# Optimization experiments

Hardware: AMD Instinct MI355X
Metric: run time of the kernel (lower is better)

Reference implementation:

```python
import jax, jax.numpy as jnp
import numpy as np

N = 50000        # nodes
E = 1000000      # edges
HID = 128        # hidden_dim
EA = 16          # edge_attr_dim
MLP_IN = 2 * HID + EA + 1   # dist + feat[row] + feat[col] + edge_attr = 273
WNUM = 3         # FullyConnectedTensorProduct(sh, 1x0e, sh) weight_numel = max_ell+1

# map each of the 9 SH components (l=0,1,2) to its l-path weight index
_L_IDX = jnp.array([0, 1, 1, 1, 2, 2, 2, 2, 2])


def _sh_lmax2(u):
    """e3nn real spherical harmonics, lmax=2, normalization='norm'.
    u: [E,3] unit vectors (e3nn x,y,z order); each l-block has unit L2 norm."""
    x, y, z = u[..., 0], u[..., 1], u[..., 2]
    s3 = jnp.sqrt(jnp.asarray(3.0, u.dtype))
    return jnp.stack([
        jnp.ones_like(x),                      # l=0
        x, y, z,                               # l=1 (unit vector)
        s3 * x * z,                            # l=2 (component / sqrt(5))
        s3 * x * y,
        y * y - 0.5 * (x * x + z * z),
        s3 * y * z,
        0.5 * s3 * (z * z - x * x),
    ], axis=-1)


def setup_inputs() -> dict:
    key = jax.random.key(0)
    ks = jax.random.split(key, 6)
    return {
        "node_feat": jax.random.normal(ks[0], (N, HID), jnp.float32),
        "node_pos": jax.random.normal(ks[1], (N, 3), jnp.float32),
        "edge_attr": jax.random.normal(ks[2], (E, EA), jnp.float32),
        "W1": jax.random.normal(ks[3], (MLP_IN, HID), jnp.float32) / np.sqrt(MLP_IN).astype(np.float32),
        "b1": jnp.zeros((HID,), jnp.float32),
        "W2": jax.random.normal(ks[4], (HID, WNUM), jnp.float32) / np.sqrt(HID).astype(np.float32),
        "b2": jnp.zeros((WNUM,), jnp.float32),
        "edge_index": jax.random.randint(ks[5], (2, E), 0, N),
    }


def reference(node_feat, node_pos, edge_attr, W1, b1, W2, b2, edge_index):
    row, col = edge_index[0], edge_index[1]
    diff = node_pos[row] - node_pos[col]                         # [E,3] gather
    dist = jnp.linalg.norm(diff, axis=-1, keepdims=True)         # [E,1]
    msg = jnp.concatenate([dist, node_feat[row], node_feat[col], edge_attr], axis=-1)
    h = jax.nn.silu(msg @ W1 + b1)                               # [E,HID]
    w = jax.nn.silu(h @ W2 + b2)                                 # [E,3] per-l TP weights (last_act=True)
    u = diff / jnp.maximum(dist, 1e-12)                          # normalize=True
    sh = jax.lax.stop_gradient(_sh_lmax2(u))                     # [E,9], .detach() in source
    # FullyConnectedTensorProduct(sh, ones '1x0e') with component irrep-norm and
    # element path-norm reduces exactly to scaling each l-block by its path weight.
    diff_sh = sh * w[:, _L_IDX]                                  # [E,9]
    # scatter-mean over destination `row`
    seg = jax.ops.segment_sum(diff_sh, row, num_segments=N)      # [N,9]
    cnt = jax.ops.segment_sum(jnp.ones((diff_sh.shape[0],), diff_sh.dtype), row, num_segments=N)
    return seg / jnp.maximum(cnt, 1.0)[:, None]
```

## Files before the change

kernel.cpp:

```cpp
#include <hip/hip_runtime.h>
#include <hip/hip_bf16.h>
#include <hip/hip_fp16.h>
#include <math.h>

#define HID 128
#define EA 16
#define BM 64
#define EAP 40
#define PQP 136
#define FTP 136
#define KT1 9
#define NC 8
#define NTHREADS 256
#define GRIDM 1536

#define HIST_OFF   0
#define WRPTR_OFF  (256*1024)
#define W1S_OFF    (512*1024)
#define W1S_ELEMS  (KT1 * NC * 64 * 8)
#define W2S_OFF    (W1S_OFF + W1S_ELEMS * 2)
#define W2S_ELEMS  (4 * 64 * 8)
#define SORTED_OFF (1024*1024)
#define FEAT16_OFF (SORTED_OFF + 8*1024*1024)
#define P_OFF      (FEAT16_OFF + 13*1024*1024)
#define Q_OFF      (P_OFF + 13*1024*1024)

typedef _Float16 half8 __attribute__((ext_vector_type(8)));
typedef _Float16 half4v __attribute__((ext_vector_type(4)));
typedef float floatx4 __attribute__((ext_vector_type(4)));
typedef unsigned long long u64;

__device__ __forceinline__ float silu_f(float x) {
    return x * (1.0f / (1.0f + __expf(-x)));
}

__global__ void prep_kernel(const float* __restrict__ W1,
                            const float* __restrict__ W2,
                            const float* __restrict__ node_feat,
                            _Float16* __restrict__ w1s,
                            _Float16* __restrict__ w2s,
                            _Float16* __restrict__ feat16,
                            float* __restrict__ seg,
                            int nf8, int nseg) {
    const int idx = blockIdx.x * NTHREADS + threadIdx.x;
    if (idx < W1S_ELEMS) {
        const int i    = idx & 7;
        const int lane = (idx >> 3) & 63;
        const int c    = (idx >> 9) & 7;
        const int kt   = idx >> 12;
        const int k    = kt * 32 + (lane >> 4) * 8 + i;
        const int n    = c * 16 + (lane & 15);
        float v = 0.0f;
        if (k < 273) {
            const int src = (k < 272) ? (k + 1) : 0;
            v = W1[src * HID + n];
        }
        w1s[idx] = (_Float16)v;
    }
    if (idx < W2S_ELEMS) {
        const int i    = idx & 7;
        const int lane = (idx >> 3) & 63;
        const int kt   = idx >> 9;
        const int k    = kt * 32 + (lane >> 4) * 8 + i;
        const int n    = lane & 15;
        const float v  = (n < 3) ? W2[k * 3 + n] : 0.0f;
        w2s[idx] = (_Float16)v;
    }
    if (idx < nf8) {
        const float4* src = (const float4*)node_feat;
        const float4 a = src[2 * idx];
        const float4 b = src[2 * idx + 1];
        half8 h = { (_Float16)a.x, (_Float16)a.y, (_Float16)a.z, (_Float16)a.w,
                    (_Float16)b.x, (_Float16)b.y, (_Float16)b.z, (_Float16)b.w };
        ((half8*)feat16)[idx] = h;
    }
    if (idx < nseg) seg[idx] = 0.0f;
}

__global__ void pq_kernel(const _Float16* __restrict__ feat16,
                          const _Float16* __restrict__ w1s,
                          _Float16* __restrict__ P,
                          _Float16* __restrict__ Q, int N) {
    __shared__ _Float16 ftile[BM][FTP];
    const int tid  = threadIdx.x;
    const int base = blockIdx.x * BM;
    const int m    = tid >> 2;
    const int sub  = tid & 3;
    const int node = base + m;
    const int ncl  = node < N ? node : 0;

    const half8* fr = (const half8*)(feat16 + (long)ncl * HID);
    #pragma unroll
    for (int t = 0; t < 4; ++t)
        *(half8*)(&ftile[m][sub * 32 + t * 8]) = fr[sub * 4 + t];
    __syncthreads();

    const int wave = tid >> 6, lane = tid & 63, lrow = lane & 15, g = lane >> 4;
    floatx4 aP[4][2], aQ[4][2];
    #pragma unroll
    for (int rb = 0; rb < 4; ++rb) {
        aP[rb][0] = (floatx4){0,0,0,0}; aP[rb][1] = (floatx4){0,0,0,0};
        aQ[rb][0] = (floatx4){0,0,0,0}; aQ[rb][1] = (floatx4){0,0,0,0};
    }
    #pragma unroll
    for (int kt = 0; kt < 4; ++kt) {
        const half8 bP0 = *(const half8*)(w1s + ((size_t)(((kt    ) * NC + 2*wave    ) * 64 + lane)) * 8);
        const half8 bP1 = *(const half8*)(w1s + ((size_t)(((kt    ) * NC + 2*wave + 1) * 64 + lane)) * 8);
        const half8 bQ0 = *(const half8*)(w1s + ((size_t)(((kt + 4) * NC + 2*wave    ) * 64 + lane)) * 8);
        const half8 bQ1 = *(const half8*)(w1s + ((size_t)(((kt + 4) * NC + 2*wave + 1) * 64 + lane)) * 8);
        #pragma unroll
        for (int rb = 0; rb < 4; ++rb) {
            const half8 af = *(const half8*)&ftile[16*rb + lrow][kt*32 + g*8];
            aP[rb][0] = __builtin_amdgcn_mfma_f32_16x16x32_f16(af, bP0, aP[rb][0], 0, 0, 0);
            aP[rb][1] = __builtin_amdgcn_mfma_f32_16x16x32_f16(af, bP1, aP[rb][1], 0, 0, 0);
            aQ[rb][0] = __builtin_amdgcn_mfma_f32_16x16x32_f16(af, bQ0, aQ[rb][0], 0, 0, 0);
            aQ[rb][1] = __builtin_amdgcn_mfma_f32_16x16x32_f16(af, bQ1, aQ[rb][1], 0, 0, 0);
        }
    }
    const int c0 = 32 * wave + lrow, c1 = c0 + 16;

    __syncthreads();
    #pragma unroll
    for (int rb = 0; rb < 4; ++rb)
        #pragma unroll
        for (int reg = 0; reg < 4; ++reg) {
            const int r = 16*rb + 4*g + reg;
            ftile[r][c0] = (_Float16)aP[rb][0][reg];
            ftile[r][c1] = (_Float16)aP[rb][1][reg];
        }
    __syncthreads();
    if (node < N) {
        #pragma unroll
        for (int t = 0; t < 4; ++t)
            *(half8*)(P + (long)node * HID + sub * 32 + t * 8) = *(half8*)&ftile[m][sub*32 + t*8];
    }
    __syncthreads();
    #pragma unroll
    for (int rb = 0; rb < 4; ++rb)
        #pragma unroll
        for (int reg = 0; reg < 4; ++reg) {
            const int r = 16*rb + 4*g + reg;
            ftile[r][c0] = (_Float16)aQ[rb][0][reg];
            ftile[r][c1] = (_Float16)aQ[rb][1][reg];
        }
    __syncthreads();
    if (node < N) {
        #pragma unroll
        for (int t = 0; t < 4; ++t)
            *(half8*)(Q + (long)node * HID + sub * 32 + t * 8) = *(half8*)&ftile[m][sub*32 + t*8];
    }
}

__global__ void hist_kernel(const int* __restrict__ edge_index,
                            int* __restrict__ hist, int E) {
    const int e = blockIdx.x * NTHREADS + threadIdx.x;
    if (e < E) atomicAdd(hist + edge_index[e], 1);
}

__global__ void scan_kernel(const int* __restrict__ hist,
                            int* __restrict__ wrptr, int N) {
    __shared__ int wsum[16];
    const int tid  = threadIdx.x;
    const int C    = (N + 1023) >> 10;
    int lo = tid * C; if (lo > N) lo = N;
    int hi = lo + C;  if (hi > N) hi = N;
    int s = 0;
    for (int i = lo; i < hi; ++i) s += hist[i];
    const int lane = tid & 63, wid = tid >> 6;
    int v = s;
    #pragma unroll
    for (int d = 1; d < 64; d <<= 1) {
        const int t = __shfl_up(v, d, 64);
        if (lane >= d) v += t;
    }
    if (lane == 63) wsum[wid] = v;
    __syncthreads();
    if (tid == 0) {
        int a = 0;
        #pragma unroll
        for (int w = 0; w < 16; ++w) { const int t = wsum[w]; wsum[w] = a; a += t; }
    }
    __syncthreads();
    int run = wsum[wid] + v - s;
    for (int i = lo; i < hi; ++i) { wrptr[i] = run; run += hist[i]; }
}

__global__ void permute_kernel(const int* __restrict__ edge_index,
                               int* __restrict__ wrptr,
                               u64* __restrict__ sorted, int E) {
    const int e = blockIdx.x * NTHREADS + threadIdx.x;
    if (e < E) {
        const int row = edge_index[e];
        const int col = edge_index[(long)E + e];
        const int p   = atomicAdd(wrptr + row, 1);
        sorted[p] = ((u64)(unsigned)e << 32)
                  | ((u64)(unsigned short)col << 16)
                  | (u64)(unsigned short)row;
    }
}

__global__ __launch_bounds__(NTHREADS, 6)
void edge_kernel(
    const _Float16* __restrict__ Pp,
    const _Float16* __restrict__ Qp,
    const float* __restrict__ node_pos,
    const float* __restrict__ edge_attr,
    const float* __restrict__ b1,
    const float* __restrict__ b2,
    const u64*   __restrict__ sorted,
    const _Float16* __restrict__ w1s,
    const _Float16* __restrict__ w2s,
    float* __restrict__ seg,
    int E, int ntiles)
{
    __shared__ _Float16 eat[BM][EAP];
    __shared__ _Float16 pq[BM][PQP];
    __shared__ float diffb[BM][4];
    __shared__ float wbuf[BM][3];
    __shared__ int   rowb[BM];

    const int tid  = threadIdx.x;
    const int m    = tid >> 2;
    const int sub  = tid & 3;
    const int wave = tid >> 6;
    const int lane = tid & 63;
    const int lrow = lane & 15;
    const int g    = lane >> 4;

    const half8 bW0 = *(const half8*)(w1s + ((size_t)((8 * NC + 2*wave    ) * 64 + lane)) * 8);
    const half8 bW1 = *(const half8*)(w1s + ((size_t)((8 * NC + 2*wave + 1) * 64 + lane)) * 8);
    const int col0 = 32 * wave + lrow, col1 = col0 + 16;
    const float bb0 = b1[col0], bb1 = b1[col1];

    for (int tile = blockIdx.x; tile < ntiles; tile += GRIDM) {
        __syncthreads();

        {
            const long p  = (long)tile * BM + m;
            const long pc = p < E ? p : (long)(E - 1);
            const u64 pk  = sorted[pc];
            const int row = (int)(pk & 0xffff);
            const int cn  = (int)((pk >> 16) & 0xffff);
            const unsigned e = (unsigned)(pk >> 32);

            const half8* Pr = (const half8*)(Pp + (long)row * HID);
            const half8* Qc = (const half8*)(Qp + (long)cn * HID);
            #pragma unroll
            for (int t = 0; t < 4; ++t) {
                const half8 a = Pr[sub * 4 + t];
                const half8 b = Qc[sub * 4 + t];
                half8 r;
                #pragma unroll
                for (int j = 0; j < 8; ++j)
                    r[j] = (_Float16)((float)a[j] + (float)b[j]);
                *(half8*)(&pq[m][sub * 32 + t * 8]) = r;
            }
            const float4 ea = ((const float4*)(edge_attr + (long)e * EA))[sub];
            half4v h4 = { (_Float16)ea.x, (_Float16)ea.y, (_Float16)ea.z, (_Float16)ea.w };
            *(half4v*)(&eat[m][sub * 4]) = h4;
            if (sub == 0) {
                rowb[m] = row;
                const float dx = node_pos[row*3+0] - node_pos[cn*3+0];
                const float dy = node_pos[row*3+1] - node_pos[cn*3+1];
                const float dz = node_pos[row*3+2] - node_pos[cn*3+2];
                const float dist = sqrtf(dx*dx + dy*dy + dz*dz);
                diffb[m][0] = dx; diffb[m][1] = dy; diffb[m][2] = dz; diffb[m][3] = dist;
                half8 z = { (_Float16)dist, (_Float16)0.f, (_Float16)0.f, (_Float16)0.f,
                            (_Float16)0.f, (_Float16)0.f, (_Float16)0.f, (_Float16)0.f };
                *(half8*)(&eat[m][16]) = z;
            } else if (sub == 1) {
                half8 z = { (_Float16)0.f, (_Float16)0.f, (_Float16)0.f, (_Float16)0.f,
                            (_Float16)0.f, (_Float16)0.f, (_Float16)0.f, (_Float16)0.f };
                *(half8*)(&eat[m][24]) = z;
            }
        }
        __syncthreads();

        floatx4 acc[4][2];
        #pragma unroll
        for (int rb = 0; rb < 4; ++rb) {
            acc[rb][0] = (floatx4){0,0,0,0};
            acc[rb][1] = (floatx4){0,0,0,0};
        }
        #pragma unroll
        for (int rb = 0; rb < 4; ++rb) {
            const half8 af = *(const half8*)&eat[16*rb + lrow][g * 8];
            acc[rb][0] = __builtin_amdgcn_mfma_f32_16x16x32_f16(af, bW0, acc[rb][0], 0, 0, 0);
            acc[rb][1] = __builtin_amdgcn_mfma_f32_16x16x32_f16(af, bW1, acc[rb][1], 0, 0, 0);
        }

        #pragma unroll
        for (int rb = 0; rb < 4; ++rb)
            #pragma unroll
            for (int reg = 0; reg < 4; ++reg) {
                const int r = 16*rb + 4*g + reg;
                const float h0 = silu_f(acc[rb][0][reg] + (float)pq[r][col0] + bb0);
                const float h1 = silu_f(acc[rb][1][reg] + (float)pq[r][col1] + bb1);
                pq[r][col0] = (_Float16)h0;
                pq[r][col1] = (_Float16)h1;
            }
        __syncthreads();

        {
            floatx4 acc2 = (floatx4){0,0,0,0};
            #pragma unroll
            for (int kt = 0; kt < 4; ++kt) {
                const half8 af = *(const half8*)&pq[16*wave + lrow][kt*32 + g*8];
                const half8 bf = *(const half8*)(w2s + ((size_t)(kt * 64 + lane)) * 8);
                acc2 = __builtin_amdgcn_mfma_f32_16x16x32_f16(af, bf, acc2, 0, 0, 0);
            }
            if (lrow < 3) {
                const float bb2 = b2[lrow];
                #pragma unroll
                for (int reg = 0; reg < 4; ++reg)
                    wbuf[16*wave + 4*g + reg][lrow] = silu_f(acc2[reg] + bb2);
            }
        }
        __syncthreads();

        if (tid < BM) {
            const long p = (long)tile * BM + tid;
            const bool valid = p < E;
            int rw = valid ? rowb[tid] : -1;
            float v[9];
            if (valid) {
                const float dx = diffb[tid][0], dy = diffb[tid][1], dz = diffb[tid][2];
                const float dist = diffb[tid][3];
                const float inv = 1.0f / fmaxf(dist, 1e-12f);
                const float x = dx * inv, y = dy * inv, z = dz * inv;
                const float s3 = 1.7320508075688772f;
                const float w0 = wbuf[tid][0], w1 = wbuf[tid][1], w2v = wbuf[tid][2];
                v[0] = w0;
                v[1] = x * w1; v[2] = y * w1; v[3] = z * w1;
                v[4] = s3 * x * z * w2v;
                v[5] = s3 * x * y * w2v;
                v[6] = (y * y - 0.5f * (x * x + z * z)) * w2v;
                v[7] = s3 * y * z * w2v;
                v[8] = 0.5f * s3 * (z * z - x * x) * w2v;
            } else {
                #pragma unroll
                for (int c = 0; c < 9; ++c) v[c] = 0.0f;
            }
            const int rprev = __shfl_up(rw, 1, 64);
            int fl = (tid == 0 || rw != rprev) ? 1 : 0;
            #pragma unroll
            for (int d = 1; d < 64; d <<= 1) {
                const int fo = __shfl_up(fl, d, 64);
                #pragma unroll
                for (int c = 0; c < 9; ++c) {
                    const float vo = __shfl_up(v[c], d, 64);
                    if (tid >= d && !fl) v[c] += vo;
                }
                if (tid >= d) fl |= fo;
            }
            const int rnext = __shfl_down(rw, 1, 64);
            const bool endseg = (tid == 63) || (rw != rnext);
            if (endseg && rw >= 0) {
                float* o = seg + (long)rw * 9;
                #pragma unroll
                for (int c = 0; c < 9; ++c) atomicAdd(o + c, v[c]);
            }
        }
    }
}

__global__ void finalize_kernel(float* __restrict__ out,
                                const int* __restrict__ hist, int n_out) {
    const int i = blockIdx.x * blockDim.x + threadIdx.x;
    if (i < n_out) {
        const float c = (float)hist[i / 9];
        out[i] = out[i] / fmaxf(c, 1.0f);
    }
}

extern "C" void kernel_launch(void* const* d_in, const int* in_sizes, int n_in,
                              void* d_out, int out_size, void* d_ws, size_t ws_size,
                              hipStream_t stream) {
    const float* node_feat  = (const float*)d_in[0];
    const float* node_pos   = (const float*)d_in[1];
    const float* edge_attr  = (const float*)d_in[2];
    const float* W1         = (const float*)d_in[3];
    const float* b1         = (const float*)d_in[4];
    const float* W2         = (const float*)d_in[5];
    const float* b2         = (const float*)d_in[6];
    const int*   edge_index = (const int*)d_in[7];

    const int E = in_sizes[7] / 2;
    const int N = in_sizes[1] / 3;
    const int ntiles = (E + BM - 1) / BM;

    char* ws = (char*)d_ws;
    float*    seg    = (float*)d_out;
    int*      hist   = (int*)(ws + HIST_OFF);
    int*      wrptr  = (int*)(ws + WRPTR_OFF);
    _Float16* w1s    = (_Float16*)(ws + W1S_OFF);
    _Float16* w2s    = (_Float16*)(ws + W2S_OFF);
    u64*      sorted = (u64*)(ws + SORTED_OFF);
    _Float16* feat16 = (_Float16*)(ws + FEAT16_OFF);
    _Float16* Pp     = (_Float16*)(ws + P_OFF);
    _Float16* Qp     = (_Float16*)(ws + Q_OFF);

    hipMemsetAsync(hist, 0, (size_t)N * sizeof(int), stream);

    const int nf8 = N * HID / 8;
    int nprep = nf8 > out_size ? nf8 : out_size;
    if (nprep < W1S_ELEMS) nprep = W1S_ELEMS;
    prep_kernel<<<(nprep + NTHREADS - 1) / NTHREADS, NTHREADS, 0, stream>>>(
        W1, W2, node_feat, w1s, w2s, feat16, seg, nf8, out_size);

    hist_kernel<<<(E + NTHREADS - 1) / NTHREADS, NTHREADS, 0, stream>>>(
        edge_index, hist, E);
    scan_kernel<<<1, 1024, 0, stream>>>(hist, wrptr, N);
    permute_kernel<<<(E + NTHREADS - 1) / NTHREADS, NTHREADS, 0, stream>>>(
        edge_index, wrptr, sorted, E);

    pq_kernel<<<(N + BM - 1) / BM, NTHREADS, 0, stream>>>(feat16, w1s, Pp, Qp, N);

    edge_kernel<<<GRIDM, NTHREADS, 0, stream>>>(
        Pp, Qp, node_pos, edge_attr, b1, b2, sorted, w1s, w2s, seg, E, ntiles);

    const int nfin = (out_size + 255) / 256;
    finalize_kernel<<<nfin, 256, 0, stream>>>(seg, hist, out_size);
}
```

Before: 465.0 us.

## Fuse hist into prep, merge permute with PQ, split segment scan across waves

Folds the histogram atomics into the prep kernel and merges the permute and PQ GEMM kernels into one launch that uses block-index ranges, removing two launches. In the edge kernel, the W2 fragments are hoisted into registers, the fp16 add is vectorised, and the 9-channel segmented scan is spread across all four waves instead of only one, with about 2-3 channels per wave. Reciprocal intrinsics replace divisions in silu and normalisation. This trades some extra register and LDS pressure (a second tile in the permute/PQ kernel) and slightly lower reciprocal precision for fewer launches and more parallel scatter work.

```diff
diff --git a/kernel.cpp b/kernel.cpp
--- a/kernel.cpp
+++ b/kernel.cpp
@@ -6,9 +6,9 @@
 #define HID 128
 #define EA 16
 #define BM 64
+#define FTP 136
 #define EAP 40
 #define PQP 136
-#define FTP 136
 #define KT1 9
 #define NC 8
 #define NTHREADS 256
@@ -31,17 +31,20 @@
 typedef unsigned long long u64;
 
 __device__ __forceinline__ float silu_f(float x) {
-    return x * (1.0f / (1.0f + __expf(-x)));
-}
-
-__global__ void prep_kernel(const float* __restrict__ W1,
-                            const float* __restrict__ W2,
-                            const float* __restrict__ node_feat,
-                            _Float16* __restrict__ w1s,
-                            _Float16* __restrict__ w2s,
-                            _Float16* __restrict__ feat16,
-                            float* __restrict__ seg,
-                            int nf8, int nseg) {
+    return x * __builtin_amdgcn_rcpf(1.0f + __expf(-x));
+}
+
+__global__ __launch_bounds__(NTHREADS, 4)
+void prep_kernel(const float* __restrict__ W1,
+                 const float* __restrict__ W2,
+                 const float* __restrict__ node_feat,
+                 const int*   __restrict__ edge_index,
+                 _Float16* __restrict__ w1s,
+                 _Float16* __restrict__ w2s,
+                 _Float16* __restrict__ feat16,
+                 float* __restrict__ seg,
+                 int*   __restrict__ hist,
+                 int nf8, int nseg, int E) {
     const int idx = blockIdx.x * NTHREADS + threadIdx.x;
     if (idx < W1S_ELEMS) {
         const int i    = idx & 7;
@@ -75,93 +78,15 @@
         ((half8*)feat16)[idx] = h;
     }
     if (idx < nseg) seg[idx] = 0.0f;
-}
-
-__global__ void pq_kernel(const _Float16* __restrict__ feat16,
-                          const _Float16* __restrict__ w1s,
-                          _Float16* __restrict__ P,
-                          _Float16* __restrict__ Q, int N) {
-    __shared__ _Float16 ftile[BM][FTP];
-    const int tid  = threadIdx.x;
-    const int base = blockIdx.x * BM;
-    const int m    = tid >> 2;
-    const int sub  = tid & 3;
-    const int node = base + m;
-    const int ncl  = node < N ? node : 0;
-
-    const half8* fr = (const half8*)(feat16 + (long)ncl * HID);
-    #pragma unroll
-    for (int t = 0; t < 4; ++t)
-        *(half8*)(&ftile[m][sub * 32 + t * 8]) = fr[sub * 4 + t];
-    __syncthreads();
-
-    const int wave = tid >> 6, lane = tid & 63, lrow = lane & 15, g = lane >> 4;
-    floatx4 aP[4][2], aQ[4][2];
-    #pragma unroll
-    for (int rb = 0; rb < 4; ++rb) {
-        aP[rb][0] = (floatx4){0,0,0,0}; aP[rb][1] = (floatx4){0,0,0,0};
-        aQ[rb][0] = (floatx4){0,0,0,0}; aQ[rb][1] = (floatx4){0,0,0,0};
-    }
-    #pragma unroll
-    for (int kt = 0; kt < 4; ++kt) {
-        const half8 bP0 = *(const half8*)(w1s + ((size_t)(((kt    ) * NC + 2*wave    ) * 64 + lane)) * 8);
-        const half8 bP1 = *(const half8*)(w1s + ((size_t)(((kt    ) * NC + 2*wave + 1) * 64 + lane)) * 8);
-        const half8 bQ0 = *(const half8*)(w1s + ((size_t)(((kt + 4) * NC + 2*wave    ) * 64 + lane)) * 8);
-        const half8 bQ1 = *(const half8*)(w1s + ((size_t)(((kt + 4) * NC + 2*wave + 1) * 64 + lane)) * 8);
-        #pragma unroll
-        for (int rb = 0; rb < 4; ++rb) {
-            const half8 af = *(const half8*)&ftile[16*rb + lrow][kt*32 + g*8];
-            aP[rb][0] = __builtin_amdgcn_mfma_f32_16x16x32_f16(af, bP0, aP[rb][0], 0, 0, 0);
-            aP[rb][1] = __builtin_amdgcn_mfma_f32_16x16x32_f16(af, bP1, aP[rb][1], 0, 0, 0);
-            aQ[rb][0] = __builtin_amdgcn_mfma_f32_16x16x32_f16(af, bQ0, aQ[rb][0], 0, 0, 0);
-            aQ[rb][1] = __builtin_amdgcn_mfma_f32_16x16x32_f16(af, bQ1, aQ[rb][1], 0, 0, 0);
-        }
-    }
-    const int c0 = 32 * wave + lrow, c1 = c0 + 16;
-
-    __syncthreads();
-    #pragma unroll
-    for (int rb = 0; rb < 4; ++rb)
-        #pragma unroll
-        for (int reg = 0; reg < 4; ++reg) {
-            const int r = 16*rb + 4*g + reg;
-            ftile[r][c0] = (_Float16)aP[rb][0][reg];
-            ftile[r][c1] = (_Float16)aP[rb][1][reg];
-        }
-    __syncthreads();
-    if (node < N) {
-        #pragma unroll
-        for (int t = 0; t < 4; ++t)
-            *(half8*)(P + (long)node * HID + sub * 32 + t * 8) = *(half8*)&ftile[m][sub*32 + t*8];
-    }
-    __syncthreads();
-    #pragma unroll
-    for (int rb = 0; rb < 4; ++rb)
-        #pragma unroll
-        for (int reg = 0; reg < 4; ++reg) {
-            const int r = 16*rb + 4*g + reg;
-            ftile[r][c0] = (_Float16)aQ[rb][0][reg];
-            ftile[r][c1] = (_Float16)aQ[rb][1][reg];
-        }
-    __syncthreads();
-    if (node < N) {
-        #pragma unroll
-        for (int t = 0; t < 4; ++t)
-            *(half8*)(Q + (long)node * HID + sub * 32 + t * 8) = *(half8*)&ftile[m][sub*32 + t*8];
-    }
-}
-
-__global__ void hist_kernel(const int* __restrict__ edge_index,
-                            int* __restrict__ hist, int E) {
-    const int e = blockIdx.x * NTHREADS + threadIdx.x;
-    if (e < E) atomicAdd(hist + edge_index[e], 1);
-}
-
-__global__ void scan_kernel(const int* __restrict__ hist,
-                            int* __restrict__ wrptr, int N) {
+    if (idx < E) atomicAdd(hist + edge_index[idx], 1);
+}
+
+__global__ __launch_bounds__(1024, 1)
+void scan_kernel(const int* __restrict__ hist,
+                 int* __restrict__ wrptr, int N) {
     __shared__ int wsum[16];
-    const int tid  = threadIdx.x;
-    const int C    = (N + 1023) >> 10;
+    const int tid = threadIdx.x;
+    const int C   = (N + 1023) >> 10;
     int lo = tid * C; if (lo > N) lo = N;
     int hi = lo + C;  if (hi > N) hi = N;
     int s = 0;
@@ -185,17 +110,108 @@
     for (int i = lo; i < hi; ++i) { wrptr[i] = run; run += hist[i]; }
 }
 
-__global__ void permute_kernel(const int* __restrict__ edge_index,
-                               int* __restrict__ wrptr,
-                               u64* __restrict__ sorted, int E) {
-    const int e = blockIdx.x * NTHREADS + threadIdx.x;
-    if (e < E) {
-        const int row = edge_index[e];
-        const int col = edge_index[(long)E + e];
-        const int p   = atomicAdd(wrptr + row, 1);
-        sorted[p] = ((u64)(unsigned)e << 32)
-                  | ((u64)(unsigned short)col << 16)
-                  | (u64)(unsigned short)row;
+__global__ __launch_bounds__(NTHREADS, 2)
+void permute_pq_kernel(const int* __restrict__ edge_index,
+                       int* __restrict__ wrptr,
+                       u64* __restrict__ sorted,
+                       const _Float16* __restrict__ feat16,
+                       const _Float16* __restrict__ w1s,
+                       _Float16* __restrict__ P,
+                       _Float16* __restrict__ Q,
+                       int E, int N, int permBlocks) {
+    __shared__ _Float16 ftile[BM][FTP];
+    __shared__ _Float16 otile[BM][FTP];
+
+    if (blockIdx.x < permBlocks) {
+        const int e = blockIdx.x * NTHREADS + threadIdx.x;
+        if (e < E) {
+            const int row = edge_index[e];
+            const int col = edge_index[(long)E + e];
+            const int p   = atomicAdd(wrptr + row, 1);
+            sorted[p] = ((u64)(unsigned)e << 32)
+                      | ((u64)(unsigned short)col << 16)
+                      | (u64)(unsigned short)row;
+        }
+        return;
+    }
+
+    const int tid  = threadIdx.x;
+    const int base = (blockIdx.x - permBlocks) * BM;
+    const int m    = tid >> 2;
+    const int sub  = tid & 3;
+    const int node = base + m;
+    const int ncl  = node < N ? node : 0;
+
+    const half8* fr = (const half8*)(feat16 + (long)ncl * HID);
+    #pragma unroll
+    for (int t = 0; t < 4; ++t)
+        *(half8*)(&ftile[m][sub * 32 + t * 8]) = fr[sub * 4 + t];
+    __syncthreads();
+
+    const int wave = tid >> 6, lane = tid & 63, lrow = lane & 15, g = lane >> 4;
+    const int c0 = 32 * wave + lrow, c1 = c0 + 16;
+
+    {
+        floatx4 aP[4][2];
+        #pragma unroll
+        for (int rb = 0; rb < 4; ++rb) { aP[rb][0] = (floatx4){0,0,0,0}; aP[rb][1] = (floatx4){0,0,0,0}; }
+        #pragma unroll
+        for (int kt = 0; kt < 4; ++kt) {
+            const half8 b0 = *(const half8*)(w1s + ((size_t)((kt * NC + 2*wave    ) * 64 + lane)) * 8);
+            const half8 b1 = *(const half8*)(w1s + ((size_t)((kt * NC + 2*wave + 1) * 64 + lane)) * 8);
+            #pragma unroll
+            for (int rb = 0; rb < 4; ++rb) {
+                const half8 af = *(const half8*)&ftile[16*rb + lrow][kt*32 + g*8];
+                aP[rb][0] = __builtin_amdgcn_mfma_f32_16x16x32_f16(af, b0, aP[rb][0], 0, 0, 0);
+                aP[rb][1] = __builtin_amdgcn_mfma_f32_16x16x32_f16(af, b1, aP[rb][1], 0, 0, 0);
+            }
+        }
+        #pragma unroll
+        for (int rb = 0; rb < 4; ++rb)
+            #pragma unroll
+            for (int reg = 0; reg < 4; ++reg) {
+                const int r = 16*rb + 4*g + reg;
+                otile[r][c0] = (_Float16)aP[rb][0][reg];
+                otile[r][c1] = (_Float16)aP[rb][1][reg];
+            }
+        __syncthreads();
+        if (node < N) {
+            #pragma unroll
+            for (int t = 0; t < 4; ++t)
+                *(half8*)(P + (long)node * HID + sub * 32 + t * 8) = *(half8*)&otile[m][sub*32 + t*8];
+        }
+        __syncthreads();
+    }
+
+    {
+        floatx4 aQ[4][2];
+        #pragma unroll
+        for (int rb = 0; rb < 4; ++rb) { aQ[rb][0] = (floatx4){0,0,0,0}; aQ[rb][1] = (floatx4){0,0,0,0}; }
+        #pragma unroll
+        for (int kt = 0; kt < 4; ++kt) {
+            const half8 b0 = *(const half8*)(w1s + ((size_t)(((kt + 4) * NC + 2*wave    ) * 64 + lane)) * 8);
+            const half8 b1 = *(const half8*)(w1s + ((size_t)(((kt + 4) * NC + 2*wave + 1) * 64 + lane)) * 8);
+            #pragma unroll
+            for (int rb = 0; rb < 4; ++rb) {
+                const half8 af = *(const half8*)&ftile[16*rb + lrow][kt*32 + g*8];
+                aQ[rb][0] = __builtin_amdgcn_mfma_f32_16x16x32_f16(af, b0, aQ[rb][0], 0, 0, 0);
+                aQ[rb][1] = __builtin_amdgcn_mfma_f32_16x16x32_f16(af, b1, aQ[rb][1], 0, 0, 0);
+            }
+        }
+        #pragma unroll
+        for (int rb = 0; rb < 4; ++rb)
+            #pragma unroll
+            for (int reg = 0; reg < 4; ++reg) {
+                const int r = 16*rb + 4*g + reg;
+                otile[r][c0] = (_Float16)aQ[rb][0][reg];
+                otile[r][c1] = (_Float16)aQ[rb][1][reg];
+            }
+        __syncthreads();
+        if (node < N) {
+            #pragma unroll
+            for (int t = 0; t < 4; ++t)
+                *(half8*)(Q + (long)node * HID + sub * 32 + t * 8) = *(half8*)&otile[m][sub*32 + t*8];
+        }
     }
 }
 
@@ -229,6 +245,10 @@
 
     const half8 bW0 = *(const half8*)(w1s + ((size_t)((8 * NC + 2*wave    ) * 64 + lane)) * 8);
     const half8 bW1 = *(const half8*)(w1s + ((size_t)((8 * NC + 2*wave + 1) * 64 + lane)) * 8);
+    half8 bw2[4];
+    #pragma unroll
+    for (int kt = 0; kt < 4; ++kt)
+        bw2[kt] = *(const half8*)(w2s + ((size_t)(kt * 64 + lane)) * 8);
     const int col0 = 32 * wave + lrow, col1 = col0 + 16;
     const float bb0 = b1[col0], bb1 = b1[col1];
 
@@ -249,11 +269,7 @@
             for (int t = 0; t < 4; ++t) {
                 const half8 a = Pr[sub * 4 + t];
                 const half8 b = Qc[sub * 4 + t];
-                half8 r;
-                #pragma unroll
-                for (int j = 0; j < 8; ++j)
-                    r[j] = (_Float16)((float)a[j] + (float)b[j]);
-                *(half8*)(&pq[m][sub * 32 + t * 8]) = r;
+                *(half8*)(&pq[m][sub * 32 + t * 8]) = a + b;
             }
             const float4 ea = ((const float4*)(edge_attr + (long)e * EA))[sub];
             half4v h4 = { (_Float16)ea.x, (_Float16)ea.y, (_Float16)ea.z, (_Float16)ea.w };
@@ -306,8 +322,7 @@
             #pragma unroll
             for (int kt = 0; kt < 4; ++kt) {
                 const half8 af = *(const half8*)&pq[16*wave + lrow][kt*32 + g*8];
-                const half8 bf = *(const half8*)(w2s + ((size_t)(kt * 64 + lane)) * 8);
-                acc2 = __builtin_amdgcn_mfma_f32_16x16x32_f16(af, bf, acc2, 0, 0, 0);
+                acc2 = __builtin_amdgcn_mfma_f32_16x16x32_f16(af, bw2[kt], acc2, 0, 0, 0);
             }
             if (lrow < 3) {
                 const float bb2 = b2[lrow];
@@ -318,47 +333,56 @@
         }
         __syncthreads();
 
-        if (tid < BM) {
-            const long p = (long)tile * BM + tid;
-            const bool valid = p < E;
-            int rw = valid ? rowb[tid] : -1;
-            float v[9];
-            if (valid) {
-                const float dx = diffb[tid][0], dy = diffb[tid][1], dz = diffb[tid][2];
-                const float dist = diffb[tid][3];
-                const float inv = 1.0f / fmaxf(dist, 1e-12f);
-                const float x = dx * inv, y = dy * inv, z = dz * inv;
-                const float s3 = 1.7320508075688772f;
-                const float w0 = wbuf[tid][0], w1 = wbuf[tid][1], w2v = wbuf[tid][2];
-                v[0] = w0;
-                v[1] = x * w1; v[2] = y * w1; v[3] = z * w1;
-                v[4] = s3 * x * z * w2v;
-                v[5] = s3 * x * y * w2v;
-                v[6] = (y * y - 0.5f * (x * x + z * z)) * w2v;
-                v[7] = s3 * y * z * w2v;
-                v[8] = 0.5f * s3 * (z * z - x * x) * w2v;
+        {
+            const long p0 = (long)tile * BM;
+            const bool valid = (p0 + lane) < E;
+            int rw = valid ? rowb[lane] : -1;
+
+            const float dx = diffb[lane][0], dy = diffb[lane][1], dz = diffb[lane][2];
+            const float dist = diffb[lane][3];
+            const float inv = __builtin_amdgcn_rcpf(fmaxf(dist, 1e-12f));
+            const float x = dx * inv, y = dy * inv, z = dz * inv;
+            const float s3 = 1.7320508075688772f;
+
+            float v0, v1, v2 = 0.0f;
+            int cA, cB;
+            if (wave == 0) {
+                const float w0 = wbuf[lane][0], w2v = wbuf[lane][2];
+                v0 = w0;  v1 = s3 * x * z * w2v;  v2 = 0.5f * s3 * (z*z - x*x) * w2v;
+                cA = 0; cB = 4;
+            } else if (wave == 1) {
+                const float w1v = wbuf[lane][1], w2v = wbuf[lane][2];
+                v0 = x * w1v;  v1 = s3 * x * y * w2v;
+                cA = 1; cB = 5;
+            } else if (wave == 2) {
+                const float w1v = wbuf[lane][1], w2v = wbuf[lane][2];
+                v0 = y * w1v;  v1 = (y*y - 0.5f*(x*x + z*z)) * w2v;
+                cA = 2; cB = 6;
             } else {
-                #pragma unroll
-                for (int c = 0; c < 9; ++c) v[c] = 0.0f;
-            }
+                const float w1v = wbuf[lane][1], w2v = wbuf[lane][2];
+                v0 = z * w1v;  v1 = s3 * y * z * w2v;
+                cA = 3; cB = 7;
+            }
+            if (!valid) { v0 = 0.0f; v1 = 0.0f; v2 = 0.0f; }
+
             const int rprev = __shfl_up(rw, 1, 64);
-            int fl = (tid == 0 || rw != rprev) ? 1 : 0;
+            int fl = (lane == 0 || rw != rprev) ? 1 : 0;
             #pragma unroll
             for (int d = 1; d < 64; d <<= 1) {
-                const int fo = __shfl_up(fl, d, 64);
-                #pragma unroll
-                for (int c = 0; c < 9; ++c) {
-                    const float vo = __shfl_up(v[c], d, 64);
-                    if (tid >= d && !fl) v[c] += vo;
-                }
-                if (tid >= d) fl |= fo;
+                const int   fo = __shfl_up(fl, d, 64);
+                const float a0 = __shfl_up(v0, d, 64);
+                const float a1 = __shfl_up(v1, d, 64);
+                const float a2 = __shfl_up(v2, d, 64);
+                if (lane >= d && !fl) { v0 += a0; v1 += a1; v2 += a2; }
+                if (lane >= d) fl |= fo;
             }
             const int rnext = __shfl_down(rw, 1, 64);
-            const bool endseg = (tid == 63) || (rw != rnext);
+            const bool endseg = (lane == 63) || (rw != rnext);
             if (endseg && rw >= 0) {
                 float* o = seg + (long)rw * 9;
-                #pragma unroll
-                for (int c = 0; c < 9; ++c) atomicAdd(o + c, v[c]);
+                atomicAdd(o + cA, v0);
+                atomicAdd(o + cB, v1);
+                if (wave == 0) atomicAdd(o + 8, v2);
             }
         }
     }
@@ -405,16 +429,17 @@
     const int nf8 = N * HID / 8;
     int nprep = nf8 > out_size ? nf8 : out_size;
     if (nprep < W1S_ELEMS) nprep = W1S_ELEMS;
+    if (nprep < E) nprep = E;
     prep_kernel<<<(nprep + NTHREADS - 1) / NTHREADS, NTHREADS, 0, stream>>>(
-        W1, W2, node_feat, w1s, w2s, feat16, seg, nf8, out_size);
-
-    hist_kernel<<<(E + NTHREADS - 1) / NTHREADS, NTHREADS, 0, stream>>>(
-        edge_index, hist, E);
+        W1, W2, node_feat, edge_index, w1s, w2s, feat16, seg, hist,
+        nf8, out_size, E);
+
     scan_kernel<<<1, 1024, 0, stream>>>(hist, wrptr, N);
-    permute_kernel<<<(E + NTHREADS - 1) / NTHREADS, NTHREADS, 0, stream>>>(
-        edge_index, wrptr, sorted, E);
-
-    pq_kernel<<<(N + BM - 1) / BM, NTHREADS, 0, stream>>>(feat16, w1s, Pp, Qp, N);
+
+    const int permBlocks = (E + NTHREADS - 1) / NTHREADS;
+    const int pqBlocks   = (N + BM - 1) / BM;
+    permute_pq_kernel<<<permBlocks + pqBlocks, NTHREADS, 0, stream>>>(
+        edge_index, wrptr, sorted, feat16, w1s, Pp, Qp, E, N, permBlocks);
 
     edge_kernel<<<GRIDM, NTHREADS, 0, stream>>>(
         Pp, Qp, node_pos, edge_attr, b1, b2, sorted, w1s, w2s, seg, E, ntiles);
```

Result: no change. 466.7 us (+0.4%).
